# Performance work log

Measured on AMD Instinct MI355X. Metric: run time of the kernel, lower is better.

## Reference

```python
import jax, jax.numpy as jnp
import numpy as np

L = 12          # layers
H = 12          # heads
D = 768         # hidden
HD = 64         # head dim
FF = 3072       # ffn dim
VOCAB = 50265
MAXPOS = 2050
WINDOWS = (32, 32, 64, 64, 128, 128, 256, 256, 512, 512, 512, 512)
EPS = 1e-5


def layer_norm(x, g, b):
    mu = jnp.mean(x, axis=-1, keepdims=True)
    var = jnp.mean(jnp.square(x - mu), axis=-1, keepdims=True)
    return (x - mu) * jax.lax.rsqrt(var + EPS) * g + b


def sliding_window_attention(q, k, v, key_add, half):
    """Banded (Longformer local) attention.
    q,k,v: [B,H,S,hd]; key_add: [B,S] additive mask; window one-sided = half.
    Queries are chunked into blocks of `half`; each block's band lies inside a
    3*half key span, so we never materialize an SxS matrix."""
    B, nh, S, hd = q.shape
    nc = S // half
    w3 = 3 * half
    qc = q.reshape(B, nh, nc, half, hd) * (1.0 / jnp.sqrt(jnp.asarray(hd, q.dtype)))
    kp = jnp.pad(k, ((0, 0), (0, 0), (half, half), (0, 0)))
    vp = jnp.pad(v, ((0, 0), (0, 0), (half, half), (0, 0)))
    ap = jnp.pad(key_add, ((0, 0), (half, half)))
    idx = jnp.arange(nc)[:, None] * half + jnp.arange(w3)[None, :]  # [nc, 3h]
    kc = kp[:, :, idx]   # [B,H,nc,3h,hd]
    vc = vp[:, :, idx]
    ac = ap[:, idx]      # [B,nc,3h]
    scores = jnp.einsum('bhcqd,bhckd->bhcqk', qc, kc)
    scores = scores + ac[:, None, :, None, :]
    qpos = jnp.arange(half)[:, None]
    kpos = jnp.arange(w3)[None, :]
    band = (kpos >= qpos) & (kpos <= qpos + 2 * half)            # [half,3h]
    gk = jnp.arange(nc)[:, None] * half - half + jnp.arange(w3)[None, :]
    valid = (gk >= 0) & (gk < S)                                  # [nc,3h]
    m = band[None, :, :] & valid[:, None, :]                      # [nc,half,3h]
    scores = jnp.where(m[None, None], scores, -1e9)
    p = jax.nn.softmax(scores, axis=-1)
    out = jnp.einsum('bhcqk,bhckd->bhcqd', p, vc)
    return out.reshape(B, nh, S, hd)


def setup_inputs() -> dict:
    key = jax.random.key(0)
    ks = jax.random.split(key, 32)
    B, S = 2, 2048
    s = 0.02
    inp = {
        'ids': jax.random.randint(ks[0], (B, S), 0, VOCAB),
        'mask': jnp.ones((B, S), jnp.float32),
        'fts': jax.random.normal(ks[1], (B, 1), jnp.float32),
        'word_emb': jax.random.normal(ks[2], (VOCAB, D)) * s,
        'pos_emb': jax.random.normal(ks[3], (MAXPOS, D)) * s,
        'type_emb': jax.random.normal(ks[4], (1, D)) * s,
        'ln_emb_g': jnp.ones((D,)), 'ln_emb_b': jnp.zeros((D,)),
        'Wq': jax.random.normal(ks[5], (L, D, D)) * s, 'bq': jnp.zeros((L, D)),
        'Wk': jax.random.normal(ks[6], (L, D, D)) * s, 'bk': jnp.zeros((L, D)),
        'Wv': jax.random.normal(ks[7], (L, D, D)) * s, 'bv': jnp.zeros((L, D)),
        'Wo': jax.random.normal(ks[8], (L, D, D)) * s, 'bo': jnp.zeros((L, D)),
        'ln1_g': jnp.ones((L, D)), 'ln1_b': jnp.zeros((L, D)),
        'W1': jax.random.normal(ks[9], (L, D, FF)) * s, 'b1': jnp.zeros((L, FF)),
        'W2': jax.random.normal(ks[10], (L, FF, D)) * s, 'b2': jnp.zeros((L, D)),
        'ln2_g': jnp.ones((L, D)), 'ln2_b': jnp.zeros((L, D)),
        'Wtop': jax.random.normal(ks[11], (D + 1, 1)) * s, 'btop': jnp.zeros((1,)),
    }
    return inp


def reference(ids, mask, fts, word_emb, pos_emb, type_emb, ln_emb_g, ln_emb_b,
              Wq, bq, Wk, bk, Wv, bv, Wo, bo, ln1_g, ln1_b,
              W1, b1, W2, b2, ln2_g, ln2_b, Wtop, btop):
    B, S = ids.shape
    # RoBERTa-style positions with padding_idx=1 (mask assumed all-valid)
    pos = jnp.arange(S) + 2
    x = word_emb[ids] + pos_emb[pos][None] + type_emb[0][None, None]
    x = layer_norm(x, ln_emb_g, ln_emb_b)
    key_add = (1.0 - mask) * -1e9  # additive key padding mask [B,S]
    for i in range(L):
        half = WINDOWS[i] // 2
        q = (x @ Wq[i] + bq[i]).reshape(B, S, H, HD).transpose(0, 2, 1, 3)
        k = (x @ Wk[i] + bk[i]).reshape(B, S, H, HD).transpose(0, 2, 1, 3)
        v = (x @ Wv[i] + bv[i]).reshape(B, S, H, HD).transpose(0, 2, 1, 3)
        a = sliding_window_attention(q, k, v, key_add, half)
        a = a.transpose(0, 2, 1, 3).reshape(B, S, D)
        x = layer_norm(x + a @ Wo[i] + bo[i], ln1_g[i], ln1_b[i])
        h = jax.nn.gelu(x @ W1[i] + b1[i], approximate=False)
        x = layer_norm(x + h @ W2[i] + b2[i], ln2_g[i], ln2_b[i])
    cls = x[:, 0, :]
    out = jnp.concatenate([cls, fts], axis=1) @ Wtop + btop
    return out
```

## Files before the change

kernel.cpp:

```cpp
#include <hip/hip_runtime.h>

typedef unsigned short u16;
using short8  = __attribute__((ext_vector_type(8))) short;
using floatx4 = __attribute__((ext_vector_type(4))) float;

static const int g_halves[12] = {16,16,32,32,64,64,128,128,256,256,256,256};

__device__ __forceinline__ float bf2f(u16 u) {
  union { unsigned int i; float f; } x; x.i = ((unsigned int)u) << 16; return x.f;
}
__device__ __forceinline__ u16 f2bf(float f) {
  union { float f; unsigned int i; } x; x.f = f;
  unsigned int r = x.i + 0x7FFFu + ((x.i >> 16) & 1u);
  return (u16)(r >> 16);
}

__device__ __forceinline__ void gld_lds16(const u16* g, u16* l) {
  __builtin_amdgcn_global_load_lds(
      (const __attribute__((address_space(1))) unsigned int*)g,
      (__attribute__((address_space(3))) unsigned int*)l, 16, 0, 0);
}

__global__ __launch_bounds__(256) void transpose_cvt(
    const float* __restrict__ in, u16* __restrict__ out, int R, int C,
    size_t inZ, size_t outZ)
{
  __shared__ u16 t[32][33];
  const int tx = threadIdx.x & 31, ty = threadIdx.x >> 5;
  const size_t bi = (size_t)blockIdx.z * inZ;
  const size_t bo = (size_t)blockIdx.z * outZ;
  const int r0 = blockIdx.y * 32, c0 = blockIdx.x * 32;
#pragma unroll
  for (int j = 0; j < 32; j += 8)
    t[ty + j][tx] = f2bf(in[bi + (size_t)(r0 + ty + j) * C + (c0 + tx)]);
  __syncthreads();
#pragma unroll
  for (int j = 0; j < 32; j += 8)
    out[bo + (size_t)(c0 + ty + j) * R + (r0 + tx)] = t[tx][ty + j];
}

template<int EPI>
__global__ __launch_bounds__(256) void gemm_bt(
    const u16* __restrict__ A, const u16* __restrict__ Bt,
    const float* __restrict__ biasA, const float* __restrict__ biasB, const float* __restrict__ biasC,
    const float* __restrict__ res, float* __restrict__ outF, u16* __restrict__ outB,
    u16* __restrict__ qh, u16* __restrict__ ql, u16* __restrict__ kh, u16* __restrict__ kl,
    u16* __restrict__ vv, int M, int N, int K)
{
  __shared__ __align__(16) u16 lsA[128 * 32];
  __shared__ __align__(16) u16 lsB[128 * 32];
  const int tid  = threadIdx.x;
  const int wave = tid >> 6, lane = tid & 63;
  const int quad = lane >> 4, l16 = lane & 15;
  const int m0 = blockIdx.y * 128, n0 = blockIdx.x * 128;
  const int wm = (wave >> 1) * 64, wn = (wave & 1) * 64;
  const int srow = lane >> 2;
  const int skof = (lane & 3) * 8;

  floatx4 acc[4][4] = {};

  for (int k0 = 0; k0 < K; k0 += 32) {
    __syncthreads();
#pragma unroll
    for (int c = wave; c < 16; c += 4) {
      if (c < 8)
        gld_lds16(A  + (size_t)(m0 + c * 16 + srow) * K + k0 + skof, lsA + c * 512);
      else
        gld_lds16(Bt + (size_t)(n0 + (c - 8) * 16 + srow) * K + k0 + skof, lsB + (c - 8) * 512);
    }
    __syncthreads();
    short8 af[4], bfr[4];
#pragma unroll
    for (int i = 0; i < 4; ++i)
      af[i]  = *(const short8*)(lsA + (wm + i * 16 + l16) * 32 + quad * 8);
#pragma unroll
    for (int j = 0; j < 4; ++j)
      bfr[j] = *(const short8*)(lsB + (wn + j * 16 + l16) * 32 + quad * 8);
#pragma unroll
    for (int i = 0; i < 4; ++i)
#pragma unroll
      for (int j = 0; j < 4; ++j)
        acc[i][j] = __builtin_amdgcn_mfma_f32_16x16x32_bf16(af[i], bfr[j], acc[i][j], 0, 0, 0);
  }

#pragma unroll
  for (int i = 0; i < 4; ++i)
#pragma unroll
    for (int j = 0; j < 4; ++j) {
      const int col = n0 + wn + j * 16 + l16;
      if (EPI == 3) {
        const int seg = (col >= 1536) ? 2 : (col >= 768) ? 1 : 0;
        const int cc = col - seg * 768;
        const int hh = cc >> 6, dd = cc & 63;
        const float bvl = (seg == 0) ? biasA[cc] : (seg == 1) ? biasB[cc] : biasC[cc];
#pragma unroll
        for (int r = 0; r < 4; ++r) {
          const int row = m0 + wm + i * 16 + quad * 4 + r;
          const int bI = row >> 11, ss = row & 2047;
          const size_t ob = (((size_t)bI * 12 + hh) * 2048 + ss) * 64 + dd;
          float v = acc[i][j][r] + bvl;
          if (seg == 0) {
            v *= 0.125f;
            const u16 hi = f2bf(v);
            qh[ob] = hi; ql[ob] = f2bf(v - bf2f(hi));
          } else if (seg == 1) {
            const u16 hi = f2bf(v);
            kh[ob] = hi; kl[ob] = f2bf(v - bf2f(hi));
          } else {
            vv[ob] = f2bf(v);
          }
        }
      } else {
        const float bvl = biasA[col];
#pragma unroll
        for (int r = 0; r < 4; ++r) {
          const int row = m0 + wm + i * 16 + quad * 4 + r;
          const size_t idx = (size_t)row * N + col;
          float v = acc[i][j][r] + bvl;
          if (EPI == 1) { v += res[idx]; outF[idx] = v; }
          if (EPI == 2) {
            v = 0.5f * v * (1.0f + erff(v * 0.70710678118654752f));
            outB[idx] = f2bf(v);
          }
        }
      }
    }
}

__global__ __launch_bounds__(256) void attn_mfma(
    const u16* __restrict__ qh_g, const u16* __restrict__ ql_g,
    const u16* __restrict__ kh_g, const u16* __restrict__ kl_g,
    const u16* __restrict__ v_g,  const float* __restrict__ mask,
    u16* __restrict__ ab, int halfw)
{
  __shared__ __align__(16) u16 lsKh[2048];
  __shared__ __align__(16) u16 lsKl[2048];
  __shared__ __align__(16) u16 lsVT[2560];
  __shared__ __align__(16) u16 lsP[2560];

  const int b = blockIdx.z, h = blockIdx.y;
  const int bh = b * 12 + h;
  const int q0 = blockIdx.x * 64;
  const int tid = threadIdx.x, wave = tid >> 6, lane = tid & 63;
  const int quad = lane >> 4, l16 = lane & 15;
  const int qw0 = q0 + wave * 16;

  const size_t qrow = ((size_t)bh * 2048 + qw0 + l16) * 64 + quad * 8;
  const short8 qhf0 = *(const short8*)(qh_g + qrow);
  const short8 qhf1 = *(const short8*)(qh_g + qrow + 32);
  const short8 qlf0 = *(const short8*)(ql_g + qrow);
  const short8 qlf1 = *(const short8*)(ql_g + qrow + 32);

  floatx4 oacc[4] = {};
  float mrow[4] = {-3.0e38f, -3.0e38f, -3.0e38f, -3.0e38f};
  float lrow[4] = {0.f, 0.f, 0.f, 0.f};

  const int lo_u = (q0 - halfw > 0) ? q0 - halfw : 0;
  const int hi_u = (q0 + 63 + halfw < 2047) ? q0 + 63 + halfw : 2047;
  const int ntiles = (hi_u - lo_u + 32) >> 5;
  const int wlo = qw0 - halfw, whi = qw0 + 15 + halfw;

  u16* Pw = lsP + wave * 640;

  for (int it = 0; it < ntiles; ++it) {
    const int k0 = lo_u + it * 32;
    __syncthreads();
#pragma unroll
    for (int s2 = 0; s2 < 2; ++s2) {
      const int c = wave * 2 + s2;
      const u16* src = (c < 4) ? kh_g : kl_g;
      u16* dst = ((c < 4) ? lsKh : lsKl) + (c & 3) * 512;
      const int keyc = k0 + (c & 3) * 8;
      if (keyc + 7 < 2048) {
        gld_lds16(src + ((size_t)bh * 2048 + keyc) * 64 + lane * 8, dst);
      } else {
        const int key = keyc + (lane >> 3);
        if (key < 2048)
          *(short8*)(dst + lane * 8) =
              *(const short8*)(src + ((size_t)bh * 2048 + key) * 64 + (lane & 7) * 8);
      }
    }
    {
      const int key = tid & 31, dg = tid >> 5;
      const int gk2 = k0 + key;
      if (gk2 < 2048) {
        const short8 t8 = *(const short8*)(v_g + ((size_t)bh * 2048 + gk2) * 64 + dg * 8);
#pragma unroll
        for (int e = 0; e < 8; ++e) lsVT[(dg * 8 + e) * 40 + key] = (u16)t8[e];
      } else {
#pragma unroll
        for (int e = 0; e < 8; ++e) lsVT[(dg * 8 + e) * 40 + key] = 0;
      }
    }
    __syncthreads();
    if (k0 + 31 < wlo || k0 > whi) continue;

    floatx4 sc[2];
#pragma unroll
    for (int ct = 0; ct < 2; ++ct) {
      const u16* kb = lsKh + (ct * 16 + l16) * 64 + quad * 8;
      const u16* lb = lsKl + (ct * 16 + l16) * 64 + quad * 8;
      const short8 kh0 = *(const short8*)(kb);
      const short8 kh1 = *(const short8*)(kb + 32);
      const short8 kl0 = *(const short8*)(lb);
      const short8 kl1 = *(const short8*)(lb + 32);
      floatx4 sa = {};
      sa = __builtin_amdgcn_mfma_f32_16x16x32_bf16(qhf0, kh0, sa, 0, 0, 0);
      sa = __builtin_amdgcn_mfma_f32_16x16x32_bf16(qhf1, kh1, sa, 0, 0, 0);
      sa = __builtin_amdgcn_mfma_f32_16x16x32_bf16(qlf0, kh0, sa, 0, 0, 0);
      sa = __builtin_amdgcn_mfma_f32_16x16x32_bf16(qlf1, kh1, sa, 0, 0, 0);
      sa = __builtin_amdgcn_mfma_f32_16x16x32_bf16(qhf0, kl0, sa, 0, 0, 0);
      sa = __builtin_amdgcn_mfma_f32_16x16x32_bf16(qhf1, kl1, sa, 0, 0, 0);
      sc[ct] = sa;
    }
#pragma unroll
    for (int ct = 0; ct < 2; ++ct) {
      const int g = k0 + ct * 16 + l16;
      const int gc = (g < 2047) ? g : 2047;
      const float ma = (1.0f - mask[b * 2048 + gc]) * -1.0e9f;
#pragma unroll
      for (int r = 0; r < 4; ++r) {
        const int t = qw0 + quad * 4 + r;
        const bool valid = (g >= t - halfw) && (g <= t + halfw) && (g < 2048);
        sc[ct][r] = valid ? sc[ct][r] + ma : -1.0e9f;
      }
    }
    float pr[2][4];
#pragma unroll
    for (int r = 0; r < 4; ++r) {
      float rm = fmaxf(sc[0][r], sc[1][r]);
      rm = fmaxf(rm, __shfl_xor(rm, 1, 64));
      rm = fmaxf(rm, __shfl_xor(rm, 2, 64));
      rm = fmaxf(rm, __shfl_xor(rm, 4, 64));
      rm = fmaxf(rm, __shfl_xor(rm, 8, 64));
      const float mn = fmaxf(mrow[r], rm);
      const float al = __expf(mrow[r] - mn);
      mrow[r] = mn;
      const float p0 = __expf(sc[0][r] - mn);
      const float p1 = __expf(sc[1][r] - mn);
      pr[0][r] = p0; pr[1][r] = p1;
      float rs = p0 + p1;
      rs += __shfl_xor(rs, 1, 64);
      rs += __shfl_xor(rs, 2, 64);
      rs += __shfl_xor(rs, 4, 64);
      rs += __shfl_xor(rs, 8, 64);
      lrow[r] = lrow[r] * al + rs;
#pragma unroll
      for (int dt = 0; dt < 4; ++dt) oacc[dt][r] *= al;
    }
#pragma unroll
    for (int ct = 0; ct < 2; ++ct)
#pragma unroll
      for (int r = 0; r < 4; ++r)
        Pw[(quad * 4 + r) * 40 + ct * 16 + l16] = f2bf(pr[ct][r]);
    const short8 pa = *(const short8*)(Pw + l16 * 40 + quad * 8);
#pragma unroll
    for (int dt = 0; dt < 4; ++dt) {
      const short8 vf = *(const short8*)(lsVT + (dt * 16 + l16) * 40 + quad * 8);
      oacc[dt] = __builtin_amdgcn_mfma_f32_16x16x32_bf16(pa, vf, oacc[dt], 0, 0, 0);
    }
  }

#pragma unroll
  for (int r = 0; r < 4; ++r) {
    const float inv = 1.0f / lrow[r];
    const size_t orow = ((size_t)b * 2048 + qw0 + quad * 4 + r) * 768 + h * 64;
#pragma unroll
    for (int dt = 0; dt < 4; ++dt)
      ab[orow + dt * 16 + l16] = f2bf(oacc[dt][r] * inv);
  }
}

__global__ __launch_bounds__(256) void embed_ln_kernel(
    const int* __restrict__ ids, const float* __restrict__ wemb, const float* __restrict__ pemb,
    const float* __restrict__ temb, const float* __restrict__ g, const float* __restrict__ be,
    float* __restrict__ x, u16* __restrict__ xb)
{
  const int t = blockIdx.x;
  const int s = t & 2047;
  const int id = ids[t];
  const int tid = threadIdx.x;
  const int wave = tid >> 6, lane = tid & 63;

  float vals[3]; float sum = 0.f, ssq = 0.f;
#pragma unroll
  for (int i = 0; i < 3; ++i) {
    const int d = tid + i * 256;
    const float v = wemb[(size_t)id * 768 + d] + pemb[(size_t)(s + 2) * 768 + d] + temb[d];
    vals[i] = v; sum += v; ssq += v * v;
  }
#pragma unroll
  for (int off = 32; off; off >>= 1) { sum += __shfl_xor(sum, off, 64); ssq += __shfl_xor(ssq, off, 64); }
  __shared__ float rb[8];
  if (lane == 0) { rb[wave] = sum; rb[4 + wave] = ssq; }
  __syncthreads();
  sum = rb[0] + rb[1] + rb[2] + rb[3];
  ssq = rb[4] + rb[5] + rb[6] + rb[7];
  const float mu = sum * (1.f / 768.f);
  const float var = ssq * (1.f / 768.f) - mu * mu;
  const float rstd = rsqrtf(var + 1e-5f);
#pragma unroll
  for (int i = 0; i < 3; ++i) {
    const int d = tid + i * 256;
    const float o = (vals[i] - mu) * rstd * g[d] + be[d];
    x[(size_t)t * 768 + d] = o;
    xb[(size_t)t * 768 + d] = f2bf(o);
  }
}

__global__ __launch_bounds__(256) void ln_kernel(
    const float* __restrict__ y, const float* __restrict__ g, const float* __restrict__ be,
    float* __restrict__ x, u16* __restrict__ xb)
{
  const int t = blockIdx.x;
  const int tid = threadIdx.x;
  const int wave = tid >> 6, lane = tid & 63;
  const float* yr = y + (size_t)t * 768;

  float vals[3]; float sum = 0.f, ssq = 0.f;
#pragma unroll
  for (int i = 0; i < 3; ++i) {
    const float v = yr[tid + i * 256];
    vals[i] = v; sum += v; ssq += v * v;
  }
#pragma unroll
  for (int off = 32; off; off >>= 1) { sum += __shfl_xor(sum, off, 64); ssq += __shfl_xor(ssq, off, 64); }
  __shared__ float rb[8];
  if (lane == 0) { rb[wave] = sum; rb[4 + wave] = ssq; }
  __syncthreads();
  sum = rb[0] + rb[1] + rb[2] + rb[3];
  ssq = rb[4] + rb[5] + rb[6] + rb[7];
  const float mu = sum * (1.f / 768.f);
  const float var = ssq * (1.f / 768.f) - mu * mu;
  const float rstd = rsqrtf(var + 1e-5f);
#pragma unroll
  for (int i = 0; i < 3; ++i) {
    const int d = tid + i * 256;
    const float o = (vals[i] - mu) * rstd * g[d] + be[d];
    x[(size_t)t * 768 + d] = o;
    xb[(size_t)t * 768 + d] = f2bf(o);
  }
}

__global__ __launch_bounds__(256) void head_kernel(
    const float* __restrict__ x, const float* __restrict__ fts,
    const float* __restrict__ wtop, const float* __restrict__ btop, float* __restrict__ out)
{
  const int tid = threadIdx.x;
  const int wave = tid >> 6, lane = tid & 63;
  __shared__ float rb[4];
  for (int b = 0; b < 2; ++b) {
    float s = 0.f;
    for (int d = tid; d < 768; d += 256)
      s += x[(size_t)b * 2048 * 768 + d] * wtop[d];
#pragma unroll
    for (int off = 32; off; off >>= 1) s += __shfl_xor(s, off, 64);
    if (lane == 0) rb[wave] = s;
    __syncthreads();
    if (tid == 0) {
      float r = rb[0] + rb[1] + rb[2] + rb[3];
      r += fts[b] * wtop[768] + btop[0];
      out[b] = r;
    }
    __syncthreads();
  }
}

extern "C" void kernel_launch(void* const* d_in, const int* in_sizes, int n_in,
                              void* d_out, int out_size, void* d_ws, size_t ws_size,
                              hipStream_t stream)
{
  const int*   ids  = (const int*)d_in[0];
  const float* mask = (const float*)d_in[1];
  const float* fts  = (const float*)d_in[2];
  const float* wemb = (const float*)d_in[3];
  const float* pemb = (const float*)d_in[4];
  const float* temb = (const float*)d_in[5];
  const float* lneg = (const float*)d_in[6];
  const float* lneb = (const float*)d_in[7];
  const float* Wq   = (const float*)d_in[8];
  const float* bq   = (const float*)d_in[9];
  const float* Wk   = (const float*)d_in[10];
  const float* bk   = (const float*)d_in[11];
  const float* Wv   = (const float*)d_in[12];
  const float* bvv  = (const float*)d_in[13];
  const float* Wo   = (const float*)d_in[14];
  const float* bo   = (const float*)d_in[15];
  const float* ln1g = (const float*)d_in[16];
  const float* ln1b = (const float*)d_in[17];
  const float* W1   = (const float*)d_in[18];
  const float* b1   = (const float*)d_in[19];
  const float* W2   = (const float*)d_in[20];
  const float* b2   = (const float*)d_in[21];
  const float* ln2g = (const float*)d_in[22];
  const float* ln2b = (const float*)d_in[23];
  const float* wtop = (const float*)d_in[24];
  const float* btop = (const float*)d_in[25];

  const size_t SQ   = 768 * 768;
  const size_t SQ3  = 2304 * 768;
  const size_t SF   = 3072 * 768;
  const size_t perL = SQ3 + SQ + 2 * SF;
  const size_t NTOK = 4096;
  const size_t HDSZ = (size_t)2 * 12 * 2048 * 64;

  const size_t fixedBytes =
      NTOK * 768 * 4
    + NTOK * 768 * 2
    + NTOK * 768 * 4
    + NTOK * 768 * 2
    + NTOK * 3072 * 2
    + 5 * HDSZ * 2;
  const bool batched = ws_size >= fixedBytes + 12 * perL * 2 + 65536;
  const size_t nw = batched ? 12 : 1;

  char* p = (char*)d_ws;
  u16* wTqkv = (u16*)p; p += nw * SQ3 * 2;
  u16* wTo   = (u16*)p; p += nw * SQ  * 2;
  u16* wT1   = (u16*)p; p += nw * SF  * 2;
  u16* wT2   = (u16*)p; p += nw * SF  * 2;
  float* x  = (float*)p; p += NTOK * 768 * 4;
  u16*   xb = (u16*)p;   p += NTOK * 768 * 2;
  float* y  = (float*)p; p += NTOK * 768 * 4;
  u16*   ab = (u16*)p;   p += NTOK * 768 * 2;
  u16*   hb = (u16*)p;   p += NTOK * 3072 * 2;
  u16*   qhB = (u16*)p;  p += HDSZ * 2;
  u16*   qlB = (u16*)p;  p += HDSZ * 2;
  u16*   khB = (u16*)p;  p += HDSZ * 2;
  u16*   klB = (u16*)p;  p += HDSZ * 2;
  u16*   vbB = (u16*)p;  p += HDSZ * 2;

  if (batched) {
    transpose_cvt<<<dim3(24, 24, 12), 256, 0, stream>>>(Wq, wTqkv,             768, 768,  SQ, SQ3);
    transpose_cvt<<<dim3(24, 24, 12), 256, 0, stream>>>(Wk, wTqkv + 768 * 768, 768, 768,  SQ, SQ3);
    transpose_cvt<<<dim3(24, 24, 12), 256, 0, stream>>>(Wv, wTqkv + 1536 * 768,768, 768,  SQ, SQ3);
    transpose_cvt<<<dim3(24, 24, 12), 256, 0, stream>>>(Wo, wTo, 768, 768,  SQ, SQ);
    transpose_cvt<<<dim3(96, 24, 12), 256, 0, stream>>>(W1, wT1, 768, 3072, SF, SF);
    transpose_cvt<<<dim3(24, 96, 12), 256, 0, stream>>>(W2, wT2, 3072, 768, SF, SF);
  }

  embed_ln_kernel<<<4096, 256, 0, stream>>>(ids, wemb, pemb, temb, lneg, lneb, x, xb);

  for (int i = 0; i < 12; ++i) {
    const u16 *WqkvTl, *WoTl, *W1Tl, *W2Tl;
    if (batched) {
      WqkvTl = wTqkv + (size_t)i * SQ3; WoTl = wTo + (size_t)i * SQ;
      W1Tl = wT1 + (size_t)i * SF;      W2Tl = wT2 + (size_t)i * SF;
    } else {
      transpose_cvt<<<dim3(24, 24, 1), 256, 0, stream>>>(Wq + (size_t)i * SQ, wTqkv,             768, 768, SQ, SQ3);
      transpose_cvt<<<dim3(24, 24, 1), 256, 0, stream>>>(Wk + (size_t)i * SQ, wTqkv + 768 * 768, 768, 768, SQ, SQ3);
      transpose_cvt<<<dim3(24, 24, 1), 256, 0, stream>>>(Wv + (size_t)i * SQ, wTqkv + 1536 * 768,768, 768, SQ, SQ3);
      transpose_cvt<<<dim3(24, 24, 1), 256, 0, stream>>>(Wo + (size_t)i * SQ, wTo, 768, 768, SQ, SQ);
      transpose_cvt<<<dim3(96, 24, 1), 256, 0, stream>>>(W1 + (size_t)i * SF, wT1, 768, 3072, SF, SF);
      transpose_cvt<<<dim3(24, 96, 1), 256, 0, stream>>>(W2 + (size_t)i * SF, wT2, 3072, 768, SF, SF);
      WqkvTl = wTqkv; WoTl = wTo; W1Tl = wT1; W2Tl = wT2;
    }

    gemm_bt<3><<<dim3(18, 32), 256, 0, stream>>>(
        xb, WqkvTl, bq + (size_t)i * 768, bk + (size_t)i * 768, bvv + (size_t)i * 768,
        nullptr, nullptr, nullptr, qhB, qlB, khB, klB, vbB, 4096, 2304, 768);

    attn_mfma<<<dim3(32, 12, 2), 256, 0, stream>>>(qhB, qlB, khB, klB, vbB, mask, ab, g_halves[i]);

    gemm_bt<1><<<dim3(6, 32), 256, 0, stream>>>(
        ab, WoTl, bo + (size_t)i * 768, nullptr, nullptr, x, y, nullptr,
        nullptr, nullptr, nullptr, nullptr, nullptr, 4096, 768, 768);
    ln_kernel<<<4096, 256, 0, stream>>>(y, ln1g + (size_t)i * 768, ln1b + (size_t)i * 768, x, xb);

    gemm_bt<2><<<dim3(24, 32), 256, 0, stream>>>(
        xb, W1Tl, b1 + (size_t)i * 3072, nullptr, nullptr, nullptr, nullptr, hb,
        nullptr, nullptr, nullptr, nullptr, nullptr, 4096, 3072, 768);
    gemm_bt<1><<<dim3(6, 32), 256, 0, stream>>>(
        hb, W2Tl, b2 + (size_t)i * 768, nullptr, nullptr, x, y, nullptr,
        nullptr, nullptr, nullptr, nullptr, nullptr, 4096, 768, 3072);
    ln_kernel<<<4096, 256, 0, stream>>>(y, ln2g + (size_t)i * 768, ln2b + (size_t)i * 768, x, xb);
  }

  head_kernel<<<1, 256, 0, stream>>>(x, fts, wtop, btop, (float*)d_out);
}
```

Baseline: 3.098 ms.

## Split-K the N=768 GEMMs and fuse partial reduction, bias, residual into layernorm

Result: faster. 2.656 ms (-14.3%).

```diff
diff --git a/kernel.cpp b/kernel.cpp
--- a/kernel.cpp
+++ b/kernel.cpp
@@ -43,9 +43,9 @@
 __global__ __launch_bounds__(256) void gemm_bt(
     const u16* __restrict__ A, const u16* __restrict__ Bt,
     const float* __restrict__ biasA, const float* __restrict__ biasB, const float* __restrict__ biasC,
-    const float* __restrict__ res, float* __restrict__ outF, u16* __restrict__ outB,
+    float* __restrict__ outF, u16* __restrict__ outB,
     u16* __restrict__ qh, u16* __restrict__ ql, u16* __restrict__ kh, u16* __restrict__ kl,
-    u16* __restrict__ vv, int M, int N, int K)
+    u16* __restrict__ vv, int M, int N, int K, int KC)
 {
   __shared__ __align__(16) u16 lsA[128 * 32];
   __shared__ __align__(16) u16 lsB[128 * 32];
@@ -53,13 +53,14 @@
   const int wave = tid >> 6, lane = tid & 63;
   const int quad = lane >> 4, l16 = lane & 15;
   const int m0 = blockIdx.y * 128, n0 = blockIdx.x * 128;
+  const int kz = blockIdx.z * KC;
   const int wm = (wave >> 1) * 64, wn = (wave & 1) * 64;
   const int srow = lane >> 2;
   const int skof = (lane & 3) * 8;
 
   floatx4 acc[4][4] = {};
 
-  for (int k0 = 0; k0 < K; k0 += 32) {
+  for (int k0 = kz; k0 < kz + KC; k0 += 32) {
     __syncthreads();
 #pragma unroll
     for (int c = wave; c < 16; c += 4) {
@@ -110,18 +111,21 @@
             vv[ob] = f2bf(v);
           }
         }
-      } else {
+      } else if (EPI == 2) {
         const float bvl = biasA[col];
 #pragma unroll
         for (int r = 0; r < 4; ++r) {
           const int row = m0 + wm + i * 16 + quad * 4 + r;
           const size_t idx = (size_t)row * N + col;
           float v = acc[i][j][r] + bvl;
-          if (EPI == 1) { v += res[idx]; outF[idx] = v; }
-          if (EPI == 2) {
-            v = 0.5f * v * (1.0f + erff(v * 0.70710678118654752f));
-            outB[idx] = f2bf(v);
-          }
+          v = 0.5f * v * (1.0f + erff(v * 0.70710678118654752f));
+          outB[idx] = f2bf(v);
+        }
+      } else {
+#pragma unroll
+        for (int r = 0; r < 4; ++r) {
+          const int row = m0 + wm + i * 16 + quad * 4 + r;
+          outF[((size_t)blockIdx.z * M + row) * N + col] = acc[i][j][r];
         }
       }
     }
@@ -308,19 +312,24 @@
   }
 }
 
-__global__ __launch_bounds__(256) void ln_kernel(
-    const float* __restrict__ y, const float* __restrict__ g, const float* __restrict__ be,
-    float* __restrict__ x, u16* __restrict__ xb)
+template<int NC>
+__global__ __launch_bounds__(256) void reduce_ln_kernel(
+    const float* __restrict__ pb, const float* __restrict__ bias,
+    const float* __restrict__ g, const float* __restrict__ be,
+    float* x, u16* __restrict__ xb)
 {
   const int t = blockIdx.x;
   const int tid = threadIdx.x;
   const int wave = tid >> 6, lane = tid & 63;
-  const float* yr = y + (size_t)t * 768;
 
   float vals[3]; float sum = 0.f, ssq = 0.f;
 #pragma unroll
   for (int i = 0; i < 3; ++i) {
-    const float v = yr[tid + i * 256];
+    const int d = tid + i * 256;
+    float v = x[(size_t)t * 768 + d] + bias[d];
+#pragma unroll
+    for (int c = 0; c < NC; ++c)
+      v += pb[((size_t)c * 4096 + t) * 768 + d];
     vals[i] = v; sum += v; ssq += v * v;
   }
 #pragma unroll
@@ -407,7 +416,7 @@
   const size_t fixedBytes =
       NTOK * 768 * 4
     + NTOK * 768 * 2
-    + NTOK * 768 * 4
+    + 4 * NTOK * 768 * 4
     + NTOK * 768 * 2
     + NTOK * 3072 * 2
     + 5 * HDSZ * 2;
@@ -421,7 +430,7 @@
   u16* wT2   = (u16*)p; p += nw * SF  * 2;
   float* x  = (float*)p; p += NTOK * 768 * 4;
   u16*   xb = (u16*)p;   p += NTOK * 768 * 2;
-  float* y  = (float*)p; p += NTOK * 768 * 4;
+  float* pb = (float*)p; p += 4 * NTOK * 768 * 4;
   u16*   ab = (u16*)p;   p += NTOK * 768 * 2;
   u16*   hb = (u16*)p;   p += NTOK * 3072 * 2;
   u16*   qhB = (u16*)p;  p += HDSZ * 2;
@@ -458,22 +467,25 @@
 
     gemm_bt<3><<<dim3(18, 32), 256, 0, stream>>>(
         xb, WqkvTl, bq + (size_t)i * 768, bk + (size_t)i * 768, bvv + (size_t)i * 768,
-        nullptr, nullptr, nullptr, qhB, qlB, khB, klB, vbB, 4096, 2304, 768);
+        nullptr, nullptr, qhB, qlB, khB, klB, vbB, 4096, 2304, 768, 768);
 
     attn_mfma<<<dim3(32, 12, 2), 256, 0, stream>>>(qhB, qlB, khB, klB, vbB, mask, ab, g_halves[i]);
 
-    gemm_bt<1><<<dim3(6, 32), 256, 0, stream>>>(
-        ab, WoTl, bo + (size_t)i * 768, nullptr, nullptr, x, y, nullptr,
-        nullptr, nullptr, nullptr, nullptr, nullptr, 4096, 768, 768);
-    ln_kernel<<<4096, 256, 0, stream>>>(y, ln1g + (size_t)i * 768, ln1b + (size_t)i * 768, x, xb);
+    gemm_bt<4><<<dim3(6, 32, 2), 256, 0, stream>>>(
+        ab, WoTl, nullptr, nullptr, nullptr, pb, nullptr,
+        nullptr, nullptr, nullptr, nullptr, nullptr, 4096, 768, 768, 384);
+    reduce_ln_kernel<2><<<4096, 256, 0, stream>>>(
+        pb, bo + (size_t)i * 768, ln1g + (size_t)i * 768, ln1b + (size_t)i * 768, x, xb);
 
     gemm_bt<2><<<dim3(24, 32), 256, 0, stream>>>(
-        xb, W1Tl, b1 + (size_t)i * 3072, nullptr, nullptr, nullptr, nullptr, hb,
-        nullptr, nullptr, nullptr, nullptr, nullptr, 4096, 3072, 768);
-    gemm_bt<1><<<dim3(6, 32), 256, 0, stream>>>(
-        hb, W2Tl, b2 + (size_t)i * 768, nullptr, nullptr, x, y, nullptr,
-        nullptr, nullptr, nullptr, nullptr, nullptr, 4096, 768, 3072);
-    ln_kernel<<<4096, 256, 0, stream>>>(y, ln2g + (size_t)i * 768, ln2b + (size_t)i * 768, x, xb);
+        xb, W1Tl, b1 + (size_t)i * 3072, nullptr, nullptr, nullptr, hb,
+        nullptr, nullptr, nullptr, nullptr, nullptr, 4096, 3072, 768, 768);
+
+    gemm_bt<4><<<dim3(6, 32, 4), 256, 0, stream>>>(
+        hb, W2Tl, nullptr, nullptr, nullptr, pb, nullptr,
+        nullptr, nullptr, nullptr, nullptr, nullptr, 4096, 768, 3072, 768);
+    reduce_ln_kernel<4><<<4096, 256, 0, stream>>>(
+        pb, b2 + (size_t)i * 768, ln2g + (size_t)i * 768, ln2b + (size_t)i * 768, x, xb);
   }
 
   head_kernel<<<1, 256, 0, stream>>>(x, fts, wtop, btop, (float*)d_out);
```
